# Optimization experiments

Hardware: AMD Instinct MI355X
Metric: run time of the kernel (lower is better)

The kernel has to match this reference:

```python
import jax, jax.numpy as jnp
import numpy as np

HIDDEN = 1024


def setup_inputs() -> dict:
    key = jax.random.key(0)
    ks = jax.random.split(key, 8)
    B, S, H = 64, 2048, HIDDEN
    scale = 1.0 / np.sqrt(H)
    return {
        "decoder_hidden": jax.random.normal(ks[0], (B, H), jnp.float32),
        "encoder_outputs": jax.random.normal(ks[1], (B, S, 2 * H), jnp.float32),
        "coverage": jax.random.uniform(ks[2], (B, S), jnp.float32),
        "mask": jnp.ones((B, S), jnp.int32),
        # parameters (nn.Linear weight layout: (out, in); we store transposed for x @ W)
        "W_h": jax.random.normal(ks[3], (2 * H, H), jnp.float32) * scale,
        "W_d": jax.random.normal(ks[4], (H, H), jnp.float32) * scale,
        "W_c": jax.random.normal(ks[5], (1, H), jnp.float32) * scale,
        "v": jax.random.normal(ks[6], (H, 1), jnp.float32) * scale,
    }


def reference(decoder_hidden, encoder_outputs, coverage, mask, W_h, W_d, W_c, v):
    # energy: (B, S, H) = tanh(enc@W_h + dec@W_d broadcast over S + coverage*W_c)
    enc_proj = jnp.einsum("bse,eh->bsh", encoder_outputs, W_h)
    dec_proj = (decoder_hidden @ W_d)[:, None, :]            # (B,1,H)
    cov_proj = coverage[:, :, None] * W_c[0][None, None, :]  # (B,S,H)
    energy = jnp.tanh(enc_proj + dec_proj + cov_proj)
    scores = jnp.einsum("bsh,h->bs", energy, v[:, 0])        # (B,S)
    scores = jnp.where(mask == 0, jnp.float32(-10000.0), scores)
    attn_weights = jax.nn.softmax(scores, axis=1)            # (B,S)
    coverage_new = coverage + attn_weights
    context = jnp.einsum("bs,bse->be", attn_weights, encoder_outputs)  # (B,2H)
    return (context, attn_weights, coverage_new)
```

## Files before the change

kernel.cpp:

```cpp
#include <hip/hip_runtime.h>
#include <hip/hip_bf16.h>
#include <stdint.h>

#define BATCH 64
#define SEQ   2048
#define HID   1024
#define EDIM  2048

#define BM 64
#define BN 512
#define BK 32
#define KSTEPS (EDIM / BK)
#define BS (BATCH * SEQ)

typedef __bf16 bf16x8 __attribute__((ext_vector_type(8)));
typedef float  f32x4a __attribute__((ext_vector_type(4)));

__device__ __forceinline__ unsigned short f2bf(float x) {
    __hip_bfloat16 h = __float2bfloat16(x);
    return __builtin_bit_cast(unsigned short, h);
}

__device__ __forceinline__ uint2 pack4(f32x4a f) {
    uint2 r;
    r.x = (unsigned)f2bf(f.x) | ((unsigned)f2bf(f.y) << 16);
    r.y = (unsigned)f2bf(f.z) | ((unsigned)f2bf(f.w) << 16);
    return r;
}

__device__ __forceinline__ f32x4a ntload4(const float* p) {
    return __builtin_nontemporal_load((const f32x4a*)p);
}

__device__ __forceinline__ int a_waddr(int row, int c) {
    return (row << 6) + ((c ^ (row & 6)) << 3);
}
__device__ __forceinline__ int a_raddr(int row, int g) {
    return (row << 6) + ((g ^ ((row >> 1) & 3)) << 4);
}

__global__ void wh_transpose_kernel(const float* __restrict__ Wh,
                                    unsigned short* __restrict__ Wt) {
    __shared__ float tile[32][33];
    int bx = blockIdx.x & 63;
    int by = blockIdx.x >> 6;
    int e0 = bx * 32, h0 = by * 32;
    int tx = threadIdx.x & 31, ty = threadIdx.x >> 5;
    #pragma unroll
    for (int i = 0; i < 4; ++i)
        tile[ty + 8 * i][tx] = Wh[(size_t)(e0 + ty + 8 * i) * HID + h0 + tx];
    __syncthreads();
    if (ty < 4) {
        uint4 wv;
        unsigned short* ws = (unsigned short*)&wv;
        #pragma unroll
        for (int j = 0; j < 8; ++j) ws[j] = f2bf(tile[ty * 8 + j][tx]);
        *(uint4*)&Wt[(size_t)((e0 >> 3) + ty) * 8192 + (size_t)(h0 + tx) * 8] = wv;
    }
}

__global__ void dec_proj_kernel(const float* __restrict__ dec,
                                const float* __restrict__ Wd,
                                float* __restrict__ dp) {
    int gid = blockIdx.x * 256 + threadIdx.x;
    int b = gid >> 10, h = gid & 1023;
    const float* dr = dec + b * HID;
    float acc = 0.f;
    #pragma unroll 4
    for (int k = 0; k < HID; ++k) acc = fmaf(dr[k], Wd[(size_t)k * HID + h], acc);
    dp[gid] = acc;
}

#define MFMA16(a, bfv, c) __builtin_amdgcn_mfma_f32_16x16x32_bf16(a, bfv, c, 0, 0, 0)

#define KSTEP(kk, BCUR, BNXT, CURBUF, NXTBUF)                                   \
  {                                                                             \
    if ((kk) + 1 < KSTEPS) {                                                    \
      const unsigned short* bs = bptr + (size_t)((kk) + 1) * 32768;             \
      _Pragma("unroll")                                                         \
      for (int nj = 0; nj < 4; ++nj)                                            \
        BNXT[nj] = *(const bf16x8*)(bs + nj * 128);                             \
    }                                                                           \
    __builtin_amdgcn_s_setprio(1);                                              \
    _Pragma("unroll")                                                           \
    for (int mi = 0; mi < 4; ++mi) {                                            \
      bf16x8 afr = *(const bf16x8*)(CURBUF + a_raddr(mi * 16 + c15, g4));       \
      _Pragma("unroll")                                                         \
      for (int nj = 0; nj < 4; ++nj)                                            \
        acc[mi][nj] = MFMA16(afr, BCUR[nj], acc[mi][nj]);                       \
    }                                                                           \
    __builtin_amdgcn_s_setprio(0);                                              \
    if ((kk) + 1 < KSTEPS) *(uint2*)(NXTBUF + wb) = pack4(aL);                  \
    if ((kk) + 2 < KSTEPS) aL = ntload4(ap0 + ((kk) + 2) * BK);                 \
    asm volatile("s_waitcnt lgkmcnt(0)" ::: "memory");                          \
    __builtin_amdgcn_s_barrier();                                               \
    __builtin_amdgcn_sched_barrier(0);                                          \
  }

__global__ __launch_bounds__(512, 4) void scores_kernel(
    const float* __restrict__ enc, const float* __restrict__ cov,
    const unsigned short* __restrict__ Wt, const float* __restrict__ dp,
    const float* __restrict__ Wc, const float* __restrict__ vv,
    float* __restrict__ spart_out)
{
    __shared__ char Al[2][4096];
    __shared__ float cov_s[BM];
    __shared__ float sred[BM][8];

    const int tid  = threadIdx.x;
    const int lane = tid & 63;
    const int wid  = tid >> 6;
    const int c15  = lane & 15;
    const int g4   = lane >> 4;

    const int bid  = blockIdx.x;
    const int half = bid & 1;
    const int m    = bid >> 1;
    const int b    = m >> 5;
    const int s0   = (m & 31) * BM;

    const float* Abase = enc + (size_t)(b * SEQ + s0) * EDIM;
    const int arow = tid >> 3;
    const int ac   = tid & 7;
    const float* ap0 = Abase + (size_t)arow * EDIM + ac * 4;
    const int wb = a_waddr(arow, ac);

    const unsigned short* bptr =
        Wt + (size_t)g4 * 8192 + (size_t)(half * BN + wid * 64 + c15) * 8;

    f32x4a acc[4][4];
    #pragma unroll
    for (int mi = 0; mi < 4; ++mi)
        #pragma unroll
        for (int nj = 0; nj < 4; ++nj)
            #pragma unroll
            for (int r = 0; r < 4; ++r) acc[mi][nj][r] = 0.f;

    if (tid < BM) cov_s[tid] = cov[b * SEQ + s0 + tid];

    bf16x8 bA[4], bB[4];
    f32x4a aL = ntload4(ap0);
    #pragma unroll
    for (int nj = 0; nj < 4; ++nj)
        bA[nj] = *(const bf16x8*)(bptr + nj * 128);
    *(uint2*)(Al[0] + wb) = pack4(aL);
    aL = ntload4(ap0 + BK);
    asm volatile("s_waitcnt lgkmcnt(0)" ::: "memory");
    __builtin_amdgcn_s_barrier();
    __builtin_amdgcn_sched_barrier(0);

    for (int kk2 = 0; kk2 < KSTEPS; kk2 += 2) {
        KSTEP(kk2,     bA, bB, Al[0], Al[1]);
        KSTEP(kk2 + 1, bB, bA, Al[1], Al[0]);
    }

    float spart[4][4];
    #pragma unroll
    for (int mi = 0; mi < 4; ++mi)
        #pragma unroll
        for (int r = 0; r < 4; ++r) spart[mi][r] = 0.f;

    #pragma unroll
    for (int nj = 0; nj < 4; ++nj) {
        const int h = half * BN + wid * 64 + nj * 16 + c15;
        const float dv  = dp[b * HID + h];
        const float wcv = Wc[h];
        const float vvv = vv[h];
        #pragma unroll
        for (int mi = 0; mi < 4; ++mi) {
            #pragma unroll
            for (int r = 0; r < 4; ++r) {
                const int row = mi * 16 + g4 * 4 + r;
                float pre = acc[mi][nj][r] + dv + cov_s[row] * wcv;
                float pc = fminf(pre, 20.0f);
                float e2 = __expf(2.0f * pc);
                spart[mi][r] = fmaf((e2 - 1.0f) / (e2 + 1.0f), vvv, spart[mi][r]);
            }
        }
    }
    #pragma unroll
    for (int mi = 0; mi < 4; ++mi) {
        #pragma unroll
        for (int r = 0; r < 4; ++r) {
            float x = spart[mi][r];
            x += __shfl_xor(x, 1);
            x += __shfl_xor(x, 2);
            x += __shfl_xor(x, 4);
            x += __shfl_xor(x, 8);
            if (c15 == 0) sred[mi * 16 + g4 * 4 + r][wid] = x;
        }
    }
    __syncthreads();
    if (tid < BM) {
        float s = 0.f;
        #pragma unroll
        for (int w = 0; w < 8; ++w) s += sred[tid][w];
        spart_out[(size_t)half * BS + b * SEQ + s0 + tid] = s;
    }
}

__global__ void softmax_kernel(const float* __restrict__ spart,
                               const int* __restrict__ mask,
                               const float* __restrict__ cov,
                               float* __restrict__ out)
{
    __shared__ float red[8];
    int b = blockIdx.x, tid = threadIdx.x;
    float vals[8];
    float mx = -1e30f;
    #pragma unroll
    for (int i = 0; i < 8; ++i) {
        int s = tid + i * 256;
        float sc = spart[b * SEQ + s] + spart[BS + b * SEQ + s];
        sc = (mask[b * SEQ + s] == 0) ? -10000.0f : sc;
        vals[i] = sc;
        mx = fmaxf(mx, sc);
    }
    for (int m = 1; m < 64; m <<= 1) mx = fmaxf(mx, __shfl_xor(mx, m));
    if ((tid & 63) == 0) red[tid >> 6] = mx;
    __syncthreads();
    mx = fmaxf(fmaxf(red[0], red[1]), fmaxf(red[2], red[3]));
    float sum = 0.f;
    #pragma unroll
    for (int i = 0; i < 8; ++i) { vals[i] = __expf(vals[i] - mx); sum += vals[i]; }
    for (int m = 1; m < 64; m <<= 1) sum += __shfl_xor(sum, m);
    if ((tid & 63) == 0) red[4 + (tid >> 6)] = sum;
    __syncthreads();
    sum = red[4] + red[5] + red[6] + red[7];
    float inv = 1.0f / sum;
    float* attn = out + BATCH * EDIM;
    float* covn = attn + BATCH * SEQ;
    #pragma unroll
    for (int i = 0; i < 8; ++i) {
        int s = tid + i * 256;
        float w = vals[i] * inv;
        attn[b * SEQ + s] = w;
        covn[b * SEQ + s] = cov[b * SEQ + s] + w;
    }
}

__global__ void context_partial_kernel(const float* __restrict__ enc,
                                       const float* __restrict__ attn,
                                       float* __restrict__ cpart)
{
    __shared__ float w_s[512];
    int bid = blockIdx.x;
    int sc = bid & 3;
    int e0 = ((bid >> 2) & 7) * 256;
    int b  = bid >> 5;
    int tid = threadIdx.x;
    w_s[tid] = attn[b * SEQ + sc * 512 + tid];
    w_s[tid + 256] = attn[b * SEQ + sc * 512 + 256 + tid];
    __syncthreads();
    const float* ep = enc + ((size_t)b * SEQ + sc * 512) * EDIM + e0 + tid;
    float acc = 0.f;
    #pragma unroll 8
    for (int s = 0; s < 512; ++s)
        acc = fmaf(w_s[s], __builtin_nontemporal_load(ep + (size_t)s * EDIM), acc);
    cpart[((size_t)sc * BATCH + b) * EDIM + e0 + tid] = acc;
}

__global__ void ctx_reduce_kernel(const float* __restrict__ cpart,
                                  float* __restrict__ ctx)
{
    int idx = blockIdx.x * 256 + threadIdx.x;
    ctx[idx] = cpart[idx] + cpart[BATCH * EDIM + idx] +
               cpart[2 * BATCH * EDIM + idx] + cpart[3 * BATCH * EDIM + idx];
}

extern "C" void kernel_launch(void* const* d_in, const int* in_sizes, int n_in,
                              void* d_out, int out_size, void* d_ws, size_t ws_size,
                              hipStream_t stream) {
    const float* dec  = (const float*)d_in[0];
    const float* enc  = (const float*)d_in[1];
    const float* cov  = (const float*)d_in[2];
    const int*   mask = (const int*)d_in[3];
    const float* Wh   = (const float*)d_in[4];
    const float* Wd   = (const float*)d_in[5];
    const float* Wc   = (const float*)d_in[6];
    const float* v    = (const float*)d_in[7];
    float* out = (float*)d_out;

    unsigned short* Wt = (unsigned short*)d_ws;
    float* dp    = (float*)((char*)d_ws + (size_t)HID * EDIM * 2);
    float* spart = dp + BATCH * HID;
    float* cpart = spart + 2 * BS;

    wh_transpose_kernel<<<dim3(64 * 32), dim3(256), 0, stream>>>(Wh, Wt);
    dec_proj_kernel<<<dim3(BATCH * HID / 256), dim3(256), 0, stream>>>(dec, Wd, dp);
    scores_kernel<<<dim3((BS / BM) * 2), dim3(512), 0, stream>>>(
        enc, cov, Wt, dp, Wc, v, spart);
    softmax_kernel<<<dim3(BATCH), dim3(256), 0, stream>>>(spart, mask, cov, out);
    context_partial_kernel<<<dim3(BATCH * 8 * 4), dim3(256), 0, stream>>>(
        enc, out + BATCH * EDIM, cpart);
    ctx_reduce_kernel<<<dim3(BATCH * EDIM / 256), dim3(256), 0, stream>>>(cpart, out);
}
```

Before: 985.3 us.

## Add larger-tile scores kernel for second half of batch alongside original

Adds a new scores kernel using 256x256 tiles with 64-wide K steps, a double-buffered swizzled LDS A tile and a phased load/compute schedule. It runs on batches 32-63, while the original 64x512 kernel now runs only on batches 0-31. The softmax reads two partial-score buffers for the first half and four for the second. This looks like an A/B experiment. Since the two scores kernels run back to back on the same stream, any gain depends on the new kernel's efficiency on its half, and the extra partial-score traffic adds some cost.

After: 1.031 ms. 1.05x slower.

```diff
diff --git a/kernel.cpp b/kernel.cpp
--- a/kernel.cpp
+++ b/kernel.cpp
@@ -12,6 +12,7 @@
 #define BK 32
 #define KSTEPS (EDIM / BK)
 #define BS (BATCH * SEQ)
+#define NKT 32
 
 typedef __bf16 bf16x8 __attribute__((ext_vector_type(8)));
 typedef float  f32x4a __attribute__((ext_vector_type(4)));
@@ -25,6 +26,15 @@
     uint2 r;
     r.x = (unsigned)f2bf(f.x) | ((unsigned)f2bf(f.y) << 16);
     r.y = (unsigned)f2bf(f.z) | ((unsigned)f2bf(f.w) << 16);
+    return r;
+}
+
+__device__ __forceinline__ uint4 pack8(f32x4a f0, f32x4a f1) {
+    uint4 r;
+    r.x = (unsigned)f2bf(f0.x) | ((unsigned)f2bf(f0.y) << 16);
+    r.y = (unsigned)f2bf(f0.z) | ((unsigned)f2bf(f0.w) << 16);
+    r.z = (unsigned)f2bf(f1.x) | ((unsigned)f2bf(f1.y) << 16);
+    r.w = (unsigned)f2bf(f1.z) | ((unsigned)f2bf(f1.w) << 16);
     return r;
 }
 
@@ -97,7 +107,7 @@
     __builtin_amdgcn_sched_barrier(0);                                          \
   }
 
-__global__ __launch_bounds__(512, 4) void scores_kernel(
+__global__ __launch_bounds__(512, 4) void scores_v0(
     const float* __restrict__ enc, const float* __restrict__ cov,
     const unsigned short* __restrict__ Wt, const float* __restrict__ dp,
     const float* __restrict__ Wc, const float* __restrict__ vv,
@@ -199,7 +209,158 @@
     }
 }
 
-__global__ void softmax_kernel(const float* __restrict__ spart,
+#define V1PHASE(p, ASa, ASb)                                                    \
+  {                                                                             \
+    bf16x8 afr[2][2];                                                           \
+    _Pragma("unroll")                                                           \
+    for (int i = 0; i < 2; ++i) {                                               \
+      const int row = wm * 128 + (2 * (p) + i) * 16 + c15;                      \
+      _Pragma("unroll")                                                         \
+      for (int ks = 0; ks < 2; ++ks) {                                          \
+        const int g = ks * 4 + g4;                                              \
+        afr[i][ks] = *(const bf16x8*)(Acur + row * 128 + ((g ^ (row & 7)) << 4)); \
+      }                                                                         \
+    }                                                                           \
+    asm volatile("s_waitcnt lgkmcnt(0)" ::: "memory");                          \
+    __builtin_amdgcn_sched_barrier(0);                                          \
+    __builtin_amdgcn_s_setprio(1);                                              \
+    _Pragma("unroll")                                                           \
+    for (int ks = 0; ks < 2; ++ks)                                              \
+      _Pragma("unroll")                                                         \
+      for (int i = 0; i < 2; ++i)                                               \
+        _Pragma("unroll")                                                       \
+        for (int nj = 0; nj < 4; ++nj)                                          \
+          acc[2 * (p) + i][nj] =                                                \
+              MFMA16(afr[i][ks], bfr[ks][nj], acc[2 * (p) + i][nj]);            \
+    __builtin_amdgcn_s_setprio(0);                                              \
+    if (t < NKT - 1) {                                                          \
+      const int rw = (p) * 64 + ar;                                             \
+      *(uint4*)(Anxt + rw * 128 + ((ag ^ (rw & 7)) << 4)) = pack8(ASa, ASb);    \
+      int ktl = ((p) < 2) ? (t + 1) : (t + 2);                                  \
+      if (ktl >= NKT) ktl = 0;                                                  \
+      const int rq = ((((p) < 2) ? ((p) + 2) : ((p) - 2))) * 64 + ar;           \
+      const float* ap = Abase + (size_t)rq * EDIM + ktl * 64 + ag * 8;          \
+      ASa = *(const f32x4a*)ap;                                                 \
+      ASb = *(const f32x4a*)(ap + 4);                                           \
+    }                                                                           \
+    if ((p) == 3) asm volatile("s_waitcnt lgkmcnt(0)" ::: "memory");            \
+    __builtin_amdgcn_s_barrier();                                               \
+    __builtin_amdgcn_sched_barrier(0);                                          \
+  }
+
+__global__ __launch_bounds__(512, 2) void scores_v1(
+    const float* __restrict__ enc, const float* __restrict__ cov,
+    const unsigned short* __restrict__ Wt, const float* __restrict__ dp,
+    const float* __restrict__ Wc, const float* __restrict__ vv,
+    float* __restrict__ spartB)
+{
+    extern __shared__ char smem[];
+
+    const int tid  = threadIdx.x;
+    const int lane = tid & 63;
+    const int wid  = tid >> 6;
+    const int wm   = wid >> 2;
+    const int wn   = wid & 3;
+    const int c15  = lane & 15;
+    const int g4   = lane >> 4;
+
+    const int nt = blockIdx.x & 3;
+    const int mt = 256 + (blockIdx.x >> 2);
+    const int b  = mt >> 3;
+    const int s0 = (mt & 7) * 256;
+
+    const float* Abase = enc + (size_t)(b * SEQ + s0) * EDIM;
+    const int ar = tid >> 3;
+    const int ag = tid & 7;
+
+    const unsigned short* Bbase =
+        Wt + (size_t)g4 * 8192 + (size_t)(nt * 256 + wn * 64 + c15) * 8;
+
+    f32x4a acc[8][4];
+    #pragma unroll
+    for (int mi = 0; mi < 8; ++mi)
+        #pragma unroll
+        for (int nj = 0; nj < 4; ++nj)
+            #pragma unroll
+            for (int r = 0; r < 4; ++r) acc[mi][nj][r] = 0.f;
+
+    #pragma unroll
+    for (int q = 0; q < 4; ++q) {
+        const int r = q * 64 + ar;
+        const float* ap = Abase + (size_t)r * EDIM + ag * 8;
+        f32x4a t0 = *(const f32x4a*)ap;
+        f32x4a t1 = *(const f32x4a*)(ap + 4);
+        *(uint4*)(smem + r * 128 + ((ag ^ (r & 7)) << 4)) = pack8(t0, t1);
+    }
+    f32x4a aR0a, aR0b, aR1a, aR1b;
+    {
+        const float* p0 = Abase + (size_t)ar * EDIM + 64 + ag * 8;
+        aR0a = *(const f32x4a*)p0; aR0b = *(const f32x4a*)(p0 + 4);
+        const float* p1 = Abase + (size_t)(64 + ar) * EDIM + 64 + ag * 8;
+        aR1a = *(const f32x4a*)p1; aR1b = *(const f32x4a*)(p1 + 4);
+    }
+    asm volatile("s_waitcnt lgkmcnt(0)" ::: "memory");
+    __builtin_amdgcn_s_barrier();
+    __builtin_amdgcn_sched_barrier(0);
+
+    for (int t = 0; t < NKT; ++t) {
+        char* Acur = smem + (t & 1) * 32768;
+        char* Anxt = smem + ((t & 1) ^ 1) * 32768;
+        bf16x8 bfr[2][4];
+        const unsigned short* bs = Bbase + (size_t)t * 8 * 8192;
+        #pragma unroll
+        for (int ks = 0; ks < 2; ++ks)
+            #pragma unroll
+            for (int nj = 0; nj < 4; ++nj)
+                bfr[ks][nj] = *(const bf16x8*)(bs + (size_t)ks * 4 * 8192 + nj * 128);
+
+        V1PHASE(0, aR0a, aR0b)
+        V1PHASE(1, aR1a, aR1b)
+        V1PHASE(2, aR0a, aR0b)
+        V1PHASE(3, aR1a, aR1b)
+    }
+
+    __syncthreads();
+    float* sred = (float*)smem;
+    float dpv[4], wcv[4], vvv[4];
+    #pragma unroll
+    for (int nj = 0; nj < 4; ++nj) {
+        const int h = nt * 256 + wn * 64 + nj * 16 + c15;
+        dpv[nj] = dp[b * HID + h];
+        wcv[nj] = Wc[h];
+        vvv[nj] = vv[h];
+    }
+    #pragma unroll
+    for (int mi = 0; mi < 8; ++mi) {
+        #pragma unroll
+        for (int r = 0; r < 4; ++r) {
+            const int row = wm * 128 + mi * 16 + g4 * 4 + r;
+            const float cv = cov[b * SEQ + s0 + row];
+            float x = 0.f;
+            #pragma unroll
+            for (int nj = 0; nj < 4; ++nj) {
+                float pre = acc[mi][nj][r] + dpv[nj] + cv * wcv[nj];
+                float pc = fminf(pre, 20.0f);
+                float e2 = __expf(2.0f * pc);
+                x = fmaf((e2 - 1.0f) / (e2 + 1.0f), vvv[nj], x);
+            }
+            x += __shfl_xor(x, 1);
+            x += __shfl_xor(x, 2);
+            x += __shfl_xor(x, 4);
+            x += __shfl_xor(x, 8);
+            if (c15 == 0) sred[row * 4 + wn] = x;
+        }
+    }
+    __syncthreads();
+    if (tid < 256) {
+        float s = sred[tid * 4] + sred[tid * 4 + 1] +
+                  sred[tid * 4 + 2] + sred[tid * 4 + 3];
+        spartB[(size_t)nt * BS + b * SEQ + s0 + tid] = s;
+    }
+}
+
+__global__ void softmax_kernel(const float* __restrict__ spartA,
+                               const float* __restrict__ spartB,
                                const int* __restrict__ mask,
                                const float* __restrict__ cov,
                                float* __restrict__ out)
@@ -211,7 +372,14 @@
     #pragma unroll
     for (int i = 0; i < 8; ++i) {
         int s = tid + i * 256;
-        float sc = spart[b * SEQ + s] + spart[BS + b * SEQ + s];
+        float sc;
+        if (b < 32) {
+            sc = spartA[b * SEQ + s] + spartA[BS + b * SEQ + s];
+        } else {
+            sc = spartB[b * SEQ + s] + spartB[(size_t)BS + b * SEQ + s] +
+                 spartB[2 * (size_t)BS + b * SEQ + s] +
+                 spartB[3 * (size_t)BS + b * SEQ + s];
+        }
         sc = (mask[b * SEQ + s] == 0) ? -10000.0f : sc;
         vals[i] = sc;
         mx = fmaxf(mx, sc);
@@ -282,15 +450,19 @@
     float* out = (float*)d_out;
 
     unsigned short* Wt = (unsigned short*)d_ws;
-    float* dp    = (float*)((char*)d_ws + (size_t)HID * EDIM * 2);
-    float* spart = dp + BATCH * HID;
-    float* cpart = spart + 2 * BS;
+    float* dp     = (float*)((char*)d_ws + (size_t)HID * EDIM * 2);
+    float* spartA = dp + BATCH * HID;
+    float* spartB = spartA + 2 * BS;
+    float* cpart  = spartB + 4 * BS;
+
+    (void)hipFuncSetAttribute((const void*)scores_v1,
+                              hipFuncAttributeMaxDynamicSharedMemorySize, 65536);
 
     wh_transpose_kernel<<<dim3(64 * 32), dim3(256), 0, stream>>>(Wh, Wt);
     dec_proj_kernel<<<dim3(BATCH * HID / 256), dim3(256), 0, stream>>>(dec, Wd, dp);
-    scores_kernel<<<dim3((BS / BM) * 2), dim3(512), 0, stream>>>(
-        enc, cov, Wt, dp, Wc, v, spart);
-    softmax_kernel<<<dim3(BATCH), dim3(256), 0, stream>>>(spart, mask, cov, out);
+    scores_v0<<<dim3(2048), dim3(512), 0, stream>>>(enc, cov, Wt, dp, Wc, v, spartA);
+    scores_v1<<<dim3(1024), dim3(512), 65536, stream>>>(enc, cov, Wt, dp, Wc, v, spartB);
+    softmax_kernel<<<dim3(BATCH), dim3(256), 0, stream>>>(spartA, spartB, mask, cov, out);
     context_partial_kernel<<<dim3(BATCH * 8 * 4), dim3(256), 0, stream>>>(
         enc, out + BATCH * EDIM, cpart);
     ctx_reduce_kernel<<<dim3(BATCH * EDIM / 256), dim3(256), 0, stream>>>(cpart, out);
```
